# Kernel tuning notes

Measured on AMD Instinct MI355X. Metric: run time of the kernel, lower is better.

The kernel has to match this reference:

```python
import jax, jax.numpy as jnp
import numpy as np

NEG = -1e20

def _rope(x):
    # x: (N, L, H, D). Original buffers use inv_freq over D with D/2 entries;
    # sin/cos tiled to full D to broadcast (original code's einsum was under-specified for 4D).
    L, D = x.shape[1], x.shape[3]
    inv_freq = 1.0 / (10000.0 ** (jnp.arange(0, D, 2, dtype=jnp.float32) / D))
    t = jnp.arange(L, dtype=jnp.float32)
    freqs = t[:, None] * inv_freq[None, :]            # (L, D/2)
    sin = jnp.concatenate([jnp.sin(freqs)] * 2, -1)[None, :, None, :]  # (1,L,1,D)
    cos = jnp.concatenate([jnp.cos(freqs)] * 2, -1)[None, :, None, :]
    return x * cos + jnp.flip(x, -1) * sin

def setup_inputs() -> dict:
    key = jax.random.key(0)
    ks = jax.random.split(key, 8)
    N, L, E, H = 2, 1024, 2048, 16
    D = E // H
    s = 0.02
    return {
        "values": jax.random.normal(ks[0], (N, L, E), jnp.float32),
        "keys": jax.random.normal(ks[1], (N, L, E), jnp.float32),
        "queries": jax.random.normal(ks[2], (N, L, E), jnp.float32),
        "mask": jax.random.randint(ks[3], (N, 1, L, L), 0, 2, jnp.int32),
        "Wv": jax.random.normal(ks[4], (D, D), jnp.float32) * s,
        "Wk": jax.random.normal(ks[5], (D, D), jnp.float32) * s,
        "Wq": jax.random.normal(ks[6], (D, D), jnp.float32) * s,
        "Wo": jax.random.normal(ks[7], (E, E), jnp.float32) * s,
        "bo": jnp.zeros((E,), jnp.float32),
    }

def reference(values, keys, queries, mask, Wv, Wk, Wq, Wo, bo):
    N, L, E = queries.shape
    H = 16
    D = E // H
    v = values.reshape(N, L, H, D)
    k = keys.reshape(N, L, H, D)
    q = queries.reshape(N, L, H, D)
    q = _rope(q)
    k = _rope(k)
    # per-head linears (nn.Linear: x @ W.T)
    v = jnp.einsum('nlhd,od->nlho', v, Wv)
    k = jnp.einsum('nlhd,od->nlho', k, Wk)
    q = jnp.einsum('nlhd,od->nlho', q, Wq)
    energy = jnp.einsum('nqhd,nkhd->nhqk', q, k)
    energy = jnp.where(mask == 0, NEG, energy)
    attn = jax.nn.softmax(energy / jnp.sqrt(jnp.float32(E)), axis=3)
    out = jnp.einsum('nhqk,nkhd->nqhd', attn, v).reshape(N, L, E)
    return out @ Wo.T + bo
```

## Files before the change

kernel.cpp:

```cpp
#include <hip/hip_runtime.h>

#define LQ 1024
#define EMB 2048
#define NH 16
#define HD 128
#define RSCALE 0.022097086912079608f

typedef unsigned short u16x8 __attribute__((ext_vector_type(8)));
typedef __bf16 bf16x8 __attribute__((ext_vector_type(8)));
typedef float f32x4 __attribute__((ext_vector_type(4)));
typedef short s16x4 __attribute__((ext_vector_type(4)));

typedef const __attribute__((address_space(1))) unsigned int* gas_t;
typedef __attribute__((address_space(3))) unsigned int* las_t;

__device__ __forceinline__ void glds16(const void* g, void* l){
  __builtin_amdgcn_global_load_lds((gas_t)g, (las_t)l, 16, 0, 0);
}
__device__ __forceinline__ unsigned short f2b(float f){
  unsigned int x = __float_as_uint(f);
  return (unsigned short)((x + 0x7fffu + ((x >> 16) & 1u)) >> 16);
}
__device__ __forceinline__ bf16x8 as_bf(u16x8 u){
  union { u16x8 u; bf16x8 b; } c; c.u = u; return c.b;
}
__device__ __forceinline__ f32x4 mfma16(s16x4 a, s16x4 b, f32x4 c){
  return __builtin_amdgcn_mfma_f32_16x16x16bf16_1k(a, b, c, 0, 0, 0);
}

__global__ __launch_bounds__(256) void k_prep(const float* __restrict__ Wo,
                                              unsigned short* __restrict__ Wob,
                                              const int* __restrict__ M,
                                              unsigned long long* __restrict__ Mb){
  int bx = blockIdx.x, t = threadIdx.x;
  if (bx < 4096) {
    int i = (bx * 256 + t) * 4;
    float4 f = *(const float4*)&Wo[i];
    ushort4 u;
    u.x = f2b(f.x); u.y = f2b(f.y); u.z = f2b(f.z); u.w = f2b(f.w);
    *(ushort4*)&Wob[i] = u;
  } else {
    int w_idx = (bx - 4096) * 4 + (t >> 6);
    int lane = t & 63;
    int n = w_idx >> 14, row = (w_idx >> 4) & 1023, wc = w_idx & 15;
    int v = M[(size_t)n * (LQ * LQ) + (size_t)row * LQ + wc * 64 + lane];
    unsigned long long b = __ballot(v != 0);
    if (lane == 0) Mb[w_idx] = b;
  }
}

__global__ __launch_bounds__(256) void k_proj(
    const float* __restrict__ vals, const float* __restrict__ keys,
    const float* __restrict__ qrys,
    const float* __restrict__ Wv, const float* __restrict__ Wk,
    const float* __restrict__ Wq,
    unsigned short* __restrict__ vp, unsigned short* __restrict__ kp,
    unsigned short* __restrict__ qp)
{
  __shared__ unsigned short Xs[64 * 136];
  __shared__ unsigned short Ws[128 * 136];
  __shared__ float scC[4 * 128], scS[4 * 128];
  int t = threadIdx.x;
  int which = blockIdx.y;
  const float* X; const float* W; unsigned short* OUT; bool rope;
  if (which == 0)      { X = vals; W = Wv; OUT = vp; rope = false; }
  else if (which == 1) { X = keys; W = Wk; OUT = kp; rope = true;  }
  else                 { X = qrys; W = Wq; OUT = qp; rope = true;  }
  float qs = (which == 2) ? RSCALE : 1.0f;
  int m0 = blockIdx.x * 64;

  #pragma unroll
  for (int i = 0; i < 8; ++i) {
    int ci = t + 256 * i;
    int row = ci >> 4, ch = ci & 15;
    float4 a = *(const float4*)&W[row * 128 + ch * 8];
    float4 b = *(const float4*)&W[row * 128 + ch * 8 + 4];
    u16x8 u;
    u[0]=f2b(a.x); u[1]=f2b(a.y); u[2]=f2b(a.z); u[3]=f2b(a.w);
    u[4]=f2b(b.x); u[5]=f2b(b.y); u[6]=f2b(b.z); u[7]=f2b(b.w);
    *(u16x8*)&Ws[row * 136 + ch * 8] = u;
  }
  if (rope) {
    int l0 = (blockIdx.x * 4) & 1023;
    #pragma unroll
    for (int i = 0; i < 2; ++i) {
      int idx = t + 256 * i;
      int li = idx >> 7, d = idx & 127, j = d & 63;
      float inv = 1.0f / powf(10000.0f, (float)(2 * j) * 0.0078125f);
      float ang = (float)(l0 + li) * inv;
      scC[idx] = cosf(ang);
      scS[idx] = sinf(ang);
    }
  }
  __syncthreads();
  #pragma unroll
  for (int i = 0; i < 8; ++i) {
    int fi = t + 256 * i;
    int row = fi >> 5, dq = (fi & 31) * 4;
    int gr = m0 + row;
    float4 x = *(const float4*)&X[(size_t)gr * HD + dq];
    ushort4 u;
    if (rope) {
      int li = row >> 4;
      float4 xm = *(const float4*)&X[(size_t)gr * HD + (124 - dq)];
      float4 c  = *(const float4*)&scC[li * 128 + dq];
      float4 s  = *(const float4*)&scS[li * 128 + dq];
      u.x = f2b(x.x * c.x + xm.w * s.x);
      u.y = f2b(x.y * c.y + xm.z * s.y);
      u.z = f2b(x.z * c.z + xm.y * s.z);
      u.w = f2b(x.w * c.w + xm.x * s.w);
    } else {
      u.x = f2b(x.x); u.y = f2b(x.y); u.z = f2b(x.z); u.w = f2b(x.w);
    }
    *(ushort4*)&Xs[row * 136 + dq] = u;
  }
  __syncthreads();

  int w = t >> 6, lane = t & 63, quad = lane >> 4, n16 = lane & 15;
  f32x4 of[4][2];
  #pragma unroll
  for (int a = 0; a < 4; ++a)
    { of[a][0] = (f32x4){0.f,0.f,0.f,0.f}; of[a][1] = (f32x4){0.f,0.f,0.f,0.f}; }

  #pragma unroll
  for (int kd = 0; kd < 4; ++kd) {
    bf16x8 bfr[2];
    #pragma unroll
    for (int b2 = 0; b2 < 2; ++b2)
      bfr[b2] = as_bf(*(const u16x8*)&Ws[(w * 32 + b2 * 16 + n16) * 136 + kd * 32 + quad * 8]);
    #pragma unroll
    for (int a = 0; a < 4; ++a) {
      bf16x8 af = as_bf(*(const u16x8*)&Xs[(a * 16 + n16) * 136 + kd * 32 + quad * 8]);
      of[a][0] = __builtin_amdgcn_mfma_f32_16x16x32_bf16(af, bfr[0], of[a][0], 0, 0, 0);
      of[a][1] = __builtin_amdgcn_mfma_f32_16x16x32_bf16(af, bfr[1], of[a][1], 0, 0, 0);
    }
  }

  #pragma unroll
  for (int a = 0; a < 4; ++a) {
    #pragma unroll
    for (int b2 = 0; b2 < 2; ++b2) {
      #pragma unroll
      for (int r = 0; r < 4; ++r) {
        int m = m0 + a * 16 + quad * 4 + r;
        int n = m >> 14, l = (m >> 4) & 1023, h = m & 15;
        int o = w * 32 + b2 * 16 + n16;
        OUT[(((size_t)(n * NH + h)) * LQ + l) * HD + o] = f2b(of[a][b2][r] * qs);
      }
    }
  }
}

__global__ __launch_bounds__(256) void k_vtrans(const unsigned short* __restrict__ vp,
                                                unsigned short* __restrict__ vt){
  __shared__ unsigned short Ls[64 * 136];
  int t = threadIdx.x;
  int l0 = blockIdx.x * 64;
  size_t base = (size_t)blockIdx.y * LQ * HD;
  #pragma unroll
  for (int i = 0; i < 4; ++i) {
    int ci = t + 256 * i;
    int row = ci >> 4, ch = ci & 15;
    *(u16x8*)&Ls[row * 136 + ch * 8] =
        *(const u16x8*)&vp[base + (size_t)(l0 + row) * HD + ch * 8];
  }
  __syncthreads();
  #pragma unroll
  for (int i = 0; i < 4; ++i) {
    int idx = t + 256 * i;
    int d = idx & 127, lc = idx >> 7;
    u16x8 pk;
    #pragma unroll
    for (int j = 0; j < 8; ++j) pk[j] = Ls[(lc * 8 + j) * 136 + d];
    *(u16x8*)&vt[base + (size_t)d * LQ + l0 + lc * 8] = pk;
  }
}

__global__ __launch_bounds__(256) void k_attn(
    const unsigned short* __restrict__ qp, const unsigned short* __restrict__ kp,
    const unsigned short* __restrict__ vt, const unsigned long long* __restrict__ Mb,
    unsigned short* __restrict__ ao)
{
  __shared__ unsigned short Ks[64 * 128];
  __shared__ unsigned short Vt[128 * 64];
  __shared__ float ls[4][16];
  int t = threadIdx.x, w = t >> 6, lane = t & 63, quad = lane >> 4, n16 = lane & 15;
  int bh = blockIdx.y, nIdx = bh >> 4, h = bh & 15;
  int q0 = blockIdx.x * 64;
  size_t base = (size_t)bh * LQ * HD;
  const unsigned short* Q = qp + base;
  const unsigned short* K = kp + base;
  const unsigned short* V = vt + base;

  bf16x8 qf[4];
  #pragma unroll
  for (int kd = 0; kd < 4; ++kd)
    qf[kd] = as_bf(*(const u16x8*)&Q[(size_t)(q0 + w * 16 + n16) * HD + kd * 32 + quad * 8]);

  const unsigned long long* MbRow =
      Mb + ((size_t)nIdx * LQ + q0 + w * 16 + n16) * 16;

  f32x4 of[8];
  #pragma unroll
  for (int c = 0; c < 8; ++c) of[c] = (f32x4){0.f, 0.f, 0.f, 0.f};
  float lp = 0.f;
  int ub = (t & 192);

  for (int kt = 0; kt < 16; ++kt) {
    int k0 = kt * 64;
    __syncthreads();
    #pragma unroll
    for (int i = 0; i < 4; ++i) {
      int ci = t + 256 * i;
      int krow = ci >> 4, kch = (ci & 15) ^ (krow & 7);
      glds16(&K[(size_t)(k0 + krow) * HD + kch * 8], &Ks[(ub + 256 * i) * 8]);
      int vrow = ci >> 3, vch = (ci & 7) ^ (vrow & 7);
      glds16(&V[(size_t)vrow * LQ + k0 + vch * 8], &Vt[(ub + 256 * i) * 8]);
    }
    unsigned long long mq = MbRow[kt];
    __syncthreads();

    f32x4 sf[4];
    #pragma unroll
    for (int c = 0; c < 4; ++c) sf[c] = (f32x4){0.f, 0.f, 0.f, 0.f};
    #pragma unroll
    for (int kd = 0; kd < 4; ++kd) {
      #pragma unroll
      for (int c = 0; c < 4; ++c) {
        int slot = (kd * 4 + quad) ^ (n16 & 7);
        bf16x8 kv = as_bf(*(const u16x8*)&Ks[(c * 16 + n16) * 128 + slot * 8]);
        sf[c] = __builtin_amdgcn_mfma_f32_16x16x32_bf16(kv, qf[kd], sf[c], 0, 0, 0);
      }
    }
    #pragma unroll
    for (int c = 0; c < 4; ++c) {
      s16x4 pa;
      #pragma unroll
      for (int r = 0; r < 4; ++r) {
        int bit = (int)((mq >> (c * 16 + quad * 4 + r)) & 1ull);
        float p = bit ? __expf(sf[c][r]) : 0.f;
        lp += p;
        pa[r] = (short)f2b(p);
      }
      int cc = 2 * c + (quad >> 1);
      #pragma unroll
      for (int c2 = 0; c2 < 8; ++c2) {
        int row = c2 * 16 + n16;
        int slot = cc ^ (n16 & 7);
        s16x4 vv = *(const s16x4*)&Vt[row * 64 + slot * 8 + (quad & 1) * 4];
        of[c2] = mfma16(pa, vv, of[c2]);
      }
    }
  }

  {
    float s = lp;
    s += __shfl_xor(s, 16);
    s += __shfl_xor(s, 32);
    ls[w][n16] = s;
  }
  __syncthreads();
  float linv[4];
  #pragma unroll
  for (int r = 0; r < 4; ++r) linv[r] = 1.0f / fmaxf(ls[w][quad * 4 + r], 1e-30f);

  #pragma unroll
  for (int c2 = 0; c2 < 8; ++c2) {
    #pragma unroll
    for (int r = 0; r < 4; ++r) {
      ao[((size_t)(nIdx * LQ + q0 + w * 16 + quad * 4 + r)) * EMB + h * HD + c2 * 16 + n16] =
          f2b(of[c2][r] * linv[r]);
    }
  }
}

__global__ __launch_bounds__(256) void k_outproj(
    const unsigned short* __restrict__ ao, const unsigned short* __restrict__ Wob,
    const float* __restrict__ bo, float* __restrict__ out)
{
  __shared__ unsigned short As[2][128 * 64];
  __shared__ unsigned short Bs[2][64 * 64];
  int t = threadIdx.x;
  int w = t >> 6, lane = t & 63, quad = lane >> 4, n16 = lane & 15;
  int wm = w >> 1, wo = w & 1;
  int m0 = blockIdx.x * 128, o0 = blockIdx.y * 64;
  int ub = (t & 192);

  f32x4 of[4][2];
  #pragma unroll
  for (int a = 0; a < 4; ++a)
    { of[a][0] = (f32x4){0.f,0.f,0.f,0.f}; of[a][1] = (f32x4){0.f,0.f,0.f,0.f}; }

  #pragma unroll
  for (int i = 0; i < 4; ++i) {
    int ci = t + 256 * i;
    int row = ci >> 3, ch = (ci & 7) ^ (row & 7);
    glds16(&ao[(size_t)(m0 + row) * EMB + ch * 8], &As[0][(ub + 256 * i) * 8]);
  }
  #pragma unroll
  for (int i = 0; i < 2; ++i) {
    int ci = t + 256 * i;
    int row = ci >> 3, ch = (ci & 7) ^ (row & 7);
    glds16(&Wob[(size_t)(o0 + row) * EMB + ch * 8], &Bs[0][(ub + 256 * i) * 8]);
  }

  for (int kt = 0; kt < 32; ++kt) {
    int cur = kt & 1;
    __syncthreads();
    if (kt < 31) {
      int k1 = (kt + 1) * 64;
      #pragma unroll
      for (int i = 0; i < 4; ++i) {
        int ci = t + 256 * i;
        int row = ci >> 3, ch = (ci & 7) ^ (row & 7);
        glds16(&ao[(size_t)(m0 + row) * EMB + k1 + ch * 8], &As[1 - cur][(ub + 256 * i) * 8]);
      }
      #pragma unroll
      for (int i = 0; i < 2; ++i) {
        int ci = t + 256 * i;
        int row = ci >> 3, ch = (ci & 7) ^ (row & 7);
        glds16(&Wob[(size_t)(o0 + row) * EMB + k1 + ch * 8], &Bs[1 - cur][(ub + 256 * i) * 8]);
      }
    }
    #pragma unroll
    for (int kd = 0; kd < 2; ++kd) {
      int slot0 = (kd * 4 + quad);
      bf16x8 af[4], bf[2];
      #pragma unroll
      for (int a = 0; a < 4; ++a)
        af[a] = as_bf(*(const u16x8*)&As[cur][(wm * 64 + a * 16 + n16) * 64 + (slot0 ^ (n16 & 7)) * 8]);
      #pragma unroll
      for (int b = 0; b < 2; ++b)
        bf[b] = as_bf(*(const u16x8*)&Bs[cur][(wo * 32 + b * 16 + n16) * 64 + (slot0 ^ (n16 & 7)) * 8]);
      #pragma unroll
      for (int a = 0; a < 4; ++a)
        #pragma unroll
        for (int b = 0; b < 2; ++b)
          of[a][b] = __builtin_amdgcn_mfma_f32_16x16x32_bf16(af[a], bf[b], of[a][b], 0, 0, 0);
    }
  }

  float bb[2] = { bo[o0 + wo * 32 + n16], bo[o0 + wo * 32 + 16 + n16] };
  #pragma unroll
  for (int a = 0; a < 4; ++a) {
    #pragma unroll
    for (int b = 0; b < 2; ++b) {
      #pragma unroll
      for (int r = 0; r < 4; ++r) {
        out[(size_t)(m0 + wm * 64 + a * 16 + quad * 4 + r) * EMB
            + o0 + wo * 32 + b * 16 + n16] = of[a][b][r] + bb[b];
      }
    }
  }
}

extern "C" void kernel_launch(void* const* d_in, const int* in_sizes, int n_in,
                              void* d_out, int out_size, void* d_ws, size_t ws_size,
                              hipStream_t stream) {
  (void)in_sizes; (void)n_in; (void)out_size; (void)ws_size;
  const float* vals = (const float*)d_in[0];
  const float* keys = (const float*)d_in[1];
  const float* qrys = (const float*)d_in[2];
  const int*   mask = (const int*)d_in[3];
  const float* Wv   = (const float*)d_in[4];
  const float* Wk   = (const float*)d_in[5];
  const float* Wq   = (const float*)d_in[6];
  const float* Wo   = (const float*)d_in[7];
  const float* bo   = (const float*)d_in[8];
  float* out = (float*)d_out;

  unsigned short* U  = (unsigned short*)d_ws;
  unsigned short* qp = U;
  unsigned short* kp = U + 4194304;
  unsigned short* vp = U + 8388608;
  unsigned short* vt = U + 12582912;
  unsigned short* ao = U + 16777216;
  unsigned short* Wob= U + 20971520;
  unsigned long long* Mb = (unsigned long long*)(U + 25165824);

  k_prep    <<<dim3(12288),  dim3(256), 0, stream>>>(Wo, Wob, mask, Mb);
  k_proj    <<<dim3(512, 3), dim3(256), 0, stream>>>(vals, keys, qrys, Wv, Wk, Wq,
                                                     vp, kp, qp);
  k_vtrans  <<<dim3(16, 32), dim3(256), 0, stream>>>(vp, vt);
  k_attn    <<<dim3(16, 32), dim3(256), 0, stream>>>(qp, kp, vt, Mb, ao);
  k_outproj <<<dim3(16, 32), dim3(256), 0, stream>>>(ao, Wob, bo, out);
}
```

Before: 212.7 us.

## Double-buffer K/V tiles in attention, remap blocks per XCD, add setprio

```diff
diff --git a/kernel.cpp b/kernel.cpp
--- a/kernel.cpp
+++ b/kernel.cpp
@@ -20,6 +20,9 @@
 __device__ __forceinline__ unsigned short f2b(float f){
   unsigned int x = __float_as_uint(f);
   return (unsigned short)((x + 0x7fffu + ((x >> 16) & 1u)) >> 16);
+}
+__device__ __forceinline__ short f2bs(float f){
+  union { __bf16 h; short s; } c; c.h = (__bf16)f; return c.s;
 }
 __device__ __forceinline__ bf16x8 as_bf(u16x8 u){
   union { u16x8 u; bf16x8 b; } c; c.u = u; return c.b;
@@ -181,12 +184,15 @@
     const unsigned short* __restrict__ vt, const unsigned long long* __restrict__ Mb,
     unsigned short* __restrict__ ao)
 {
-  __shared__ unsigned short Ks[64 * 128];
-  __shared__ unsigned short Vt[128 * 64];
+  __shared__ unsigned short Ks[2][64 * 128];
+  __shared__ unsigned short Vt[2][128 * 64];
   __shared__ float ls[4][16];
   int t = threadIdx.x, w = t >> 6, lane = t & 63, quad = lane >> 4, n16 = lane & 15;
-  int bh = blockIdx.y, nIdx = bh >> 4, h = bh & 15;
-  int q0 = blockIdx.x * 64;
+  int lin = blockIdx.y * gridDim.x + blockIdx.x;
+  int xcd = lin & 7, j = lin >> 3;
+  int bh = xcd + 8 * (j >> 4);
+  int q0 = (j & 15) * 64;
+  int nIdx = bh >> 4, h = bh & 15;
   size_t base = (size_t)bh * LQ * HD;
   const unsigned short* Q = qp + base;
   const unsigned short* K = kp + base;
@@ -206,50 +212,66 @@
   float lp = 0.f;
   int ub = (t & 192);
 
+  #pragma unroll
+  for (int i = 0; i < 4; ++i) {
+    int ci = t + 256 * i;
+    int krow = ci >> 4, kch = (ci & 15) ^ (krow & 7);
+    glds16(&K[(size_t)krow * HD + kch * 8], &Ks[0][(ub + 256 * i) * 8]);
+    int vrow = ci >> 3, vch = (ci & 7) ^ (vrow & 7);
+    glds16(&V[(size_t)vrow * LQ + vch * 8], &Vt[0][(ub + 256 * i) * 8]);
+  }
+
   for (int kt = 0; kt < 16; ++kt) {
-    int k0 = kt * 64;
-    __syncthreads();
-    #pragma unroll
-    for (int i = 0; i < 4; ++i) {
-      int ci = t + 256 * i;
-      int krow = ci >> 4, kch = (ci & 15) ^ (krow & 7);
-      glds16(&K[(size_t)(k0 + krow) * HD + kch * 8], &Ks[(ub + 256 * i) * 8]);
-      int vrow = ci >> 3, vch = (ci & 7) ^ (vrow & 7);
-      glds16(&V[(size_t)vrow * LQ + k0 + vch * 8], &Vt[(ub + 256 * i) * 8]);
-    }
+    int cur = kt & 1;
     unsigned long long mq = MbRow[kt];
     __syncthreads();
+    if (kt < 15) {
+      int k1 = (kt + 1) * 64;
+      #pragma unroll
+      for (int i = 0; i < 4; ++i) {
+        int ci = t + 256 * i;
+        int krow = ci >> 4, kch = (ci & 15) ^ (krow & 7);
+        glds16(&K[(size_t)(k1 + krow) * HD + kch * 8], &Ks[cur ^ 1][(ub + 256 * i) * 8]);
+        int vrow = ci >> 3, vch = (ci & 7) ^ (vrow & 7);
+        glds16(&V[(size_t)vrow * LQ + k1 + vch * 8], &Vt[cur ^ 1][(ub + 256 * i) * 8]);
+      }
+    }
+    unsigned long long msh = mq >> (quad * 4);
 
     f32x4 sf[4];
     #pragma unroll
     for (int c = 0; c < 4; ++c) sf[c] = (f32x4){0.f, 0.f, 0.f, 0.f};
+    __builtin_amdgcn_s_setprio(1);
     #pragma unroll
     for (int kd = 0; kd < 4; ++kd) {
       #pragma unroll
       for (int c = 0; c < 4; ++c) {
         int slot = (kd * 4 + quad) ^ (n16 & 7);
-        bf16x8 kv = as_bf(*(const u16x8*)&Ks[(c * 16 + n16) * 128 + slot * 8]);
+        bf16x8 kv = as_bf(*(const u16x8*)&Ks[cur][(c * 16 + n16) * 128 + slot * 8]);
         sf[c] = __builtin_amdgcn_mfma_f32_16x16x32_bf16(kv, qf[kd], sf[c], 0, 0, 0);
       }
     }
+    __builtin_amdgcn_s_setprio(0);
     #pragma unroll
     for (int c = 0; c < 4; ++c) {
       s16x4 pa;
       #pragma unroll
       for (int r = 0; r < 4; ++r) {
-        int bit = (int)((mq >> (c * 16 + quad * 4 + r)) & 1ull);
+        int bit = (int)((msh >> (c * 16 + r)) & 1ull);
         float p = bit ? __expf(sf[c][r]) : 0.f;
         lp += p;
-        pa[r] = (short)f2b(p);
+        pa[r] = f2bs(p);
       }
       int cc = 2 * c + (quad >> 1);
+      __builtin_amdgcn_s_setprio(1);
       #pragma unroll
       for (int c2 = 0; c2 < 8; ++c2) {
         int row = c2 * 16 + n16;
         int slot = cc ^ (n16 & 7);
-        s16x4 vv = *(const s16x4*)&Vt[row * 64 + slot * 8 + (quad & 1) * 4];
+        s16x4 vv = *(const s16x4*)&Vt[cur][row * 64 + slot * 8 + (quad & 1) * 4];
         of[c2] = mfma16(pa, vv, of[c2]);
       }
+      __builtin_amdgcn_s_setprio(0);
     }
   }
 
```

Result: no change. 214.5 us (+0.9%).
